# Performance work log

Hardware: AMD Instinct MI355X
Metric: run time of the kernel (lower is better)

The kernel has to match this reference:

```python
import jax, jax.numpy as jnp
import numpy as np

B, T, H = 2048, 512, 64  # batch, seq_len, hidden_size


def setup_inputs() -> dict:
    key = jax.random.key(0)
    ks = jax.random.split(key, 12)
    s = 1.0 / np.sqrt(H)  # PyTorch default uniform init bound
    u = lambda k, shape: jax.random.uniform(k, shape, jnp.float32, -s, s)
    return {
        "x": jax.random.normal(ks[0], (B, T), dtype=jnp.float32),
        # layer 0: input_size=1
        "w_ih0": u(ks[1], (4 * H, 1)),
        "w_hh0": u(ks[2], (4 * H, H)),
        "b_ih0": u(ks[3], (4 * H,)),
        "b_hh0": u(ks[4], (4 * H,)),
        # layer 1: input_size=H
        "w_ih1": u(ks[5], (4 * H, H)),
        "w_hh1": u(ks[6], (4 * H, H)),
        "b_ih1": u(ks[7], (4 * H,)),
        "b_hh1": u(ks[8], (4 * H,)),
        # final projection 64 -> 1
        "fc_w": u(ks[9], (1, H)),
        "fc_b": u(ks[10], (1,)),
    }


def _lstm_layer(x, w_ih, w_hh, b_ih, b_hh):
    """x: [B, T, D] -> hidden states [B, T, H]. PyTorch gate order i,f,g,o."""
    bsz = x.shape[0]
    # input contribution for all timesteps at once: [B, T, 4H]
    gx = jnp.einsum('btd,gd->btg', x, w_ih) + b_ih + b_hh
    gx = jnp.swapaxes(gx, 0, 1)  # time-major [T, B, 4H]

    def step(carry, g_t):
        h, c = carry
        g = g_t + h @ w_hh.T  # [B, 4H]
        i, f, gg, o = jnp.split(g, 4, axis=-1)
        i = jax.nn.sigmoid(i)
        f = jax.nn.sigmoid(f)
        gg = jnp.tanh(gg)
        o = jax.nn.sigmoid(o)
        c = f * c + i * gg
        h = o * jnp.tanh(c)
        return (h, c), h

    h0 = jnp.zeros((bsz, H), dtype=x.dtype)
    _, hs = jax.lax.scan(step, (h0, h0), gx)
    return jnp.swapaxes(hs, 0, 1)  # [B, T, H]


def reference(x, w_ih0, w_hh0, b_ih0, b_hh0, w_ih1, w_hh1, b_ih1, b_hh1, fc_w, fc_b):
    x3 = x[..., None]  # unsqueeze(2): [B, T, 1]
    h1 = _lstm_layer(x3, w_ih0, w_hh0, b_ih0, b_hh0)
    h2 = _lstm_layer(h1, w_ih1, w_hh1, b_ih1, b_hh1)
    # fc applied to last timestep of layer-2 output
    return h2[:, -1, :] @ fc_w.T + fc_b  # [B, 1]
```

## Files before the change

### kernel.cpp

```cpp
#include <hip/hip_runtime.h>

#define TLEN 512
#define HDIM 64
#define NB   8
#define NTH  512
#define GRID 256
#define XPAD 516

typedef __attribute__((ext_vector_type(8))) short bf16x8;
typedef __attribute__((ext_vector_type(4))) float f32x4;

__device__ __forceinline__ float sigm(float x){ return __fdividef(1.f, 1.f+__expf(-x)); }
__device__ __forceinline__ float tanh_(float x){ return 1.f - __fdividef(2.f, __expf(2.f*x)+1.f); }

__device__ __forceinline__ short bf16rn(float f){
    unsigned u = __float_as_uint(f);
    u = (u + 0x7FFFu + ((u >> 16) & 1u)) >> 16;
    return (short)u;
}
__device__ __forceinline__ float bf2f(short s){
    return __uint_as_float(((unsigned)(unsigned short)s) << 16);
}
__device__ __forceinline__ float bf2f_u(unsigned lo16){
    return __uint_as_float(lo16 << 16);
}

__device__ __forceinline__ void loadA(const float* __restrict__ W, int rowbase, int lane,
                                      bf16x8& hi0, bf16x8& lo0, bf16x8& hi1, bf16x8& lo1)
{
    const int row = rowbase + (lane & 15);
    const int q   = lane >> 4;
    const float* p = W + row * HDIM + q * 8;
    #pragma unroll
    for (int e = 0; e < 8; ++e) {
        const float f0 = p[e];
        const float f1 = p[32 + e];
        const short a0 = bf16rn(f0); hi0[e] = a0; lo0[e] = bf16rn(f0 - bf2f(a0));
        const short a1 = bf16rn(f1); hi1[e] = a1; lo1[e] = bf16rn(f1 - bf2f(a1));
    }
}

#define MFMA __builtin_amdgcn_mfma_f32_16x16x32_bf16

__global__ __launch_bounds__(NTH)
__attribute__((amdgpu_waves_per_eu(2, 2)))
void lstm2_ws(const float* __restrict__ x,
              const float* __restrict__ w_ih0,
              const float* __restrict__ w_hh0,
              const float* __restrict__ b_ih0,
              const float* __restrict__ b_hh0,
              const float* __restrict__ w_ih1,
              const float* __restrict__ w_hh1,
              const float* __restrict__ b_ih1,
              const float* __restrict__ b_hh1,
              const float* __restrict__ fc_w,
              const float* __restrict__ fc_b,
              float* __restrict__ out)
{
    __shared__ float xs[16 * XPAD];
    __shared__ short h1f[2][2][2][4][16][8];
    __shared__ short h2f[2][2][2][4][16][8];
    __shared__ float h2last[16][HDIM];

    const int tid  = threadIdx.x;
    const int wid  = tid >> 6;
    const int lane = tid & 63;
    const int q    = lane >> 4;
    const int r15  = lane & 15;
    const int b0   = blockIdx.x * NB;
    const bool isL0   = (wid < 4);
    const bool lohalf = (r15 < 8);

    {
        const float4* xg = (const float4*)(x + (size_t)b0 * TLEN);
        for (int idx = tid; idx < 16 * TLEN / 4; idx += NTH) {
            const int row = idx >> 7;
            const int col = idx & 127;
            *(float4*)&xs[row * XPAD + col * 4] = xg[(row & 7) * 128 + col];
        }
    }
    for (int idx = tid; idx < 8192; idx += NTH) {
        ((short*)h1f)[idx] = 0;
        ((short*)h2f)[idx] = 0;
    }

    const int w4 = isL0 ? wid : (wid - 4);
    const int U0 = w4 * 16;
    bf16x8 M0h0[4], M0l0[4], M0h1[4], M0l1[4];
    bf16x8 M1h0[4], M1l0[4], M1h1[4], M1l1[4];
    f32x4 biasv[4], wih[4];
    if (isL0) {
        #pragma unroll
        for (int g = 0; g < 4; ++g)
            loadA(w_hh0, g * 64 + U0, lane, M0h0[g], M0l0[g], M0h1[g], M0l1[g]);
        #pragma unroll
        for (int g = 0; g < 4; ++g) {
            #pragma unroll
            for (int r = 0; r < 4; ++r) {
                const int row = g * 64 + U0 + q * 4 + r;
                biasv[g][r] = b_ih0[row] + b_hh0[row];
                wih[g][r]   = w_ih0[row];
            }
        }
    } else {
        #pragma unroll
        for (int g = 0; g < 4; ++g) {
            loadA(w_ih1, g * 64 + U0, lane, M0h0[g], M0l0[g], M0h1[g], M0l1[g]);
            loadA(w_hh1, g * 64 + U0, lane, M1h0[g], M1l0[g], M1h1[g], M1l1[g]);
        }
        #pragma unroll
        for (int g = 0; g < 4; ++g) {
            #pragma unroll
            for (int r = 0; r < 4; ++r) {
                const int row = g * 64 + U0 + q * 4 + r;
                biasv[g][r] = b_ih1[row] + b_hh1[row];
                wih[g][r]   = 0.f;
            }
        }
    }
    const int kh = w4 >> 1;
    const int qp = (2 * w4 + (q >> 1)) & 3;
    const int eo = (q & 1) * 4;
    float ccA = 0.f, ccB = 0.f;
    int p = 0;

    __syncthreads();

    for (int i = 0; i <= TLEN; ++i) {
        const bool active = isL0 ? (i < TLEN) : (i >= 1);
        if (active) {
            f32x4 acc[4];
            if (isL0) {
                const bf16x8 Bh0 = *(const bf16x8*)&h1f[p][0][0][q][r15][0];
                const bf16x8 Bh1 = *(const bf16x8*)&h1f[p][0][1][q][r15][0];
                const bf16x8 Bl0 = *(const bf16x8*)&h1f[p][1][0][q][r15][0];
                const bf16x8 Bl1 = *(const bf16x8*)&h1f[p][1][1][q][r15][0];
                const float xv = xs[r15 * XPAD + i];
                #pragma unroll
                for (int g = 0; g < 4; ++g) {
                    f32x4 a = biasv[g];
                    #pragma unroll
                    for (int r = 0; r < 4; ++r) a[r] = fmaf(wih[g][r], xv, a[r]);
                    a = MFMA(M0h0[g], Bh0, a, 0, 0, 0);
                    a = MFMA(M0l0[g], Bh0, a, 0, 0, 0);
                    a = MFMA(M0h0[g], Bl0, a, 0, 0, 0);
                    f32x4 b2 = {0.f, 0.f, 0.f, 0.f};
                    b2 = MFMA(M0h1[g], Bh1, b2, 0, 0, 0);
                    b2 = MFMA(M0l1[g], Bh1, b2, 0, 0, 0);
                    b2 = MFMA(M0h1[g], Bl1, b2, 0, 0, 0);
                    #pragma unroll
                    for (int r = 0; r < 4; ++r) acc[g][r] = a[r] + b2[r];
                }
            } else {
                const bf16x8 B1h0 = *(const bf16x8*)&h1f[p][0][0][q][r15][0];
                const bf16x8 B1h1 = *(const bf16x8*)&h1f[p][0][1][q][r15][0];
                const bf16x8 B1l0 = *(const bf16x8*)&h1f[p][1][0][q][r15][0];
                const bf16x8 B1l1 = *(const bf16x8*)&h1f[p][1][1][q][r15][0];
                const bf16x8 B2h0 = *(const bf16x8*)&h2f[p][0][0][q][r15][0];
                const bf16x8 B2h1 = *(const bf16x8*)&h2f[p][0][1][q][r15][0];
                const bf16x8 B2l0 = *(const bf16x8*)&h2f[p][1][0][q][r15][0];
                const bf16x8 B2l1 = *(const bf16x8*)&h2f[p][1][1][q][r15][0];
                #pragma unroll
                for (int g = 0; g < 4; ++g) {
                    f32x4 a = biasv[g];
                    a = MFMA(M0h0[g], B1h0, a, 0, 0, 0);
                    a = MFMA(M0h1[g], B1h1, a, 0, 0, 0);
                    a = MFMA(M0l0[g], B1h0, a, 0, 0, 0);
                    a = MFMA(M0l1[g], B1h1, a, 0, 0, 0);
                    a = MFMA(M0h0[g], B1l0, a, 0, 0, 0);
                    a = MFMA(M0h1[g], B1l1, a, 0, 0, 0);
                    f32x4 h = {0.f, 0.f, 0.f, 0.f};
                    h = MFMA(M1h0[g], B2h0, h, 0, 0, 0);
                    h = MFMA(M1h1[g], B2h1, h, 0, 0, 0);
                    h = MFMA(M1l0[g], B2h0, h, 0, 0, 0);
                    h = MFMA(M1l1[g], B2h1, h, 0, 0, 0);
                    h = MFMA(M1h0[g], B2l0, h, 0, 0, 0);
                    h = MFMA(M1h1[g], B2l1, h, 0, 0, 0);
                    #pragma unroll
                    for (int r = 0; r < 4; ++r) acc[g][r] = a[r] + h[r];
                }
            }
            float a0g[4], a1g[4];
            #pragma unroll
            for (int g = 0; g < 4; ++g) {
                a0g[g] = lohalf ? acc[g][0] : acc[g][2];
                a1g[g] = lohalf ? acc[g][1] : acc[g][3];
            }
            float hvA, hvB;
            {
                const float gi = sigm(a0g[0]), gf = sigm(a0g[1]);
                const float gg = tanh_(a0g[2]), go = sigm(a0g[3]);
                ccA = fmaf(gf, ccA, gi * gg);
                hvA = go * tanh_(ccA);
            }
            {
                const float gi = sigm(a1g[0]), gf = sigm(a1g[1]);
                const float gg = tanh_(a1g[2]), go = sigm(a1g[3]);
                ccB = fmaf(gf, ccB, gi * gg);
                hvB = go * tanh_(ccB);
            }
            const short sA = bf16rn(hvA), lA = bf16rn(hvA - bf2f(sA));
            const short sB = bf16rn(hvB), lB = bf16rn(hvB - bf2f(sB));
            const unsigned ownH = (unsigned)(unsigned short)sA | ((unsigned)(unsigned short)sB << 16);
            const unsigned ownL = (unsigned)(unsigned short)lA | ((unsigned)(unsigned short)lB << 16);
            const unsigned othH = (unsigned)__shfl_xor((int)ownH, 8, 64);
            const unsigned othL = (unsigned)__shfl_xor((int)ownL, 8, 64);
            const unsigned h01 = lohalf ? ownH : othH;
            const unsigned h23 = lohalf ? othH : ownH;
            const unsigned l01 = lohalf ? ownL : othL;
            const unsigned l23 = lohalf ? othL : ownL;
            if (isL0) {
                *(uint2*)&h1f[p ^ 1][0][kh][qp][r15][eo] = (uint2){h01, h23};
                *(uint2*)&h1f[p ^ 1][1][kh][qp][r15][eo] = (uint2){l01, l23};
            } else {
                *(uint2*)&h2f[p ^ 1][0][kh][qp][r15][eo] = (uint2){h01, h23};
                *(uint2*)&h2f[p ^ 1][1][kh][qp][r15][eo] = (uint2){l01, l23};
                if (i == TLEN) {
                    f32x4 hv;
                    hv[0] = bf2f_u(h01 & 0xFFFFu) + bf2f_u(l01 & 0xFFFFu);
                    hv[1] = bf2f_u(h01 >> 16)     + bf2f_u(l01 >> 16);
                    hv[2] = bf2f_u(h23 & 0xFFFFu) + bf2f_u(l23 & 0xFFFFu);
                    hv[3] = bf2f_u(h23 >> 16)     + bf2f_u(l23 >> 16);
                    *(f32x4*)&h2last[r15][U0 + q * 4] = hv;
                }
            }
        }
        __syncthreads();
        p ^= 1;
    }

    {
        const int fb = tid >> 5, fs = tid & 31;
        float psum = fc_w[fs] * h2last[fb][fs] + fc_w[fs + 32] * h2last[fb][fs + 32];
        psum += __shfl_xor(psum, 16);
        psum += __shfl_xor(psum, 8);
        psum += __shfl_xor(psum, 4);
        psum += __shfl_xor(psum, 2);
        psum += __shfl_xor(psum, 1);
        if (fs == 0 && fb < NB) out[b0 + fb] = psum + fc_b[0];
    }
}

extern "C" void kernel_launch(void* const* d_in, const int* in_sizes, int n_in,
                              void* d_out, int out_size, void* d_ws, size_t ws_size,
                              hipStream_t stream) {
    const float* xp     = (const float*)d_in[0];
    const float* w_ih0  = (const float*)d_in[1];
    const float* w_hh0  = (const float*)d_in[2];
    const float* b_ih0  = (const float*)d_in[3];
    const float* b_hh0  = (const float*)d_in[4];
    const float* w_ih1  = (const float*)d_in[5];
    const float* w_hh1  = (const float*)d_in[6];
    const float* b_ih1  = (const float*)d_in[7];
    const float* b_hh1  = (const float*)d_in[8];
    const float* fc_w   = (const float*)d_in[9];
    const float* fc_b   = (const float*)d_in[10];
    float* outp = (float*)d_out;

    lstm2_ws<<<dim3(GRID), dim3(NTH), 0, stream>>>(
        xp, w_ih0, w_hh0, b_ih0, b_hh0,
        w_ih1, w_hh1, b_ih1, b_hh1, fc_w, fc_b, outp);
}
```

Before: 872.8 us.

## Split layer-1 input projection into separate wave group with 3-stage pipeline

Expands the block from 8 to 12 waves, organised as three groups: layer-0 recurrence, layer-1 input projection (W_ih1·h1), and layer-1 recurrence (W_hh1·h2). The input projection result passes through a double-buffered shared array one step later. This removes the critical-path imbalance where layer-1 waves did twice the MFMA work of layer-0 waves. In exchange it adds a pipeline stage (one extra timestep iteration), extra LDS traffic, and drops the waves_per_eu hint. Bias and x terms are now added after the MFMA instead of seeding the accumulator.

New measurement: 949.2 us. 8.7% more time.

```diff
diff --git a/kernel.cpp b/kernel.cpp
--- a/kernel.cpp
+++ b/kernel.cpp
@@ -3,7 +3,7 @@
 #define TLEN 512
 #define HDIM 64
 #define NB   8
-#define NTH  512
+#define NTH  768
 #define GRID 256
 #define XPAD 516
 
@@ -43,32 +43,33 @@
 #define MFMA __builtin_amdgcn_mfma_f32_16x16x32_bf16
 
 __global__ __launch_bounds__(NTH)
-__attribute__((amdgpu_waves_per_eu(2, 2)))
-void lstm2_ws(const float* __restrict__ x,
-              const float* __restrict__ w_ih0,
-              const float* __restrict__ w_hh0,
-              const float* __restrict__ b_ih0,
-              const float* __restrict__ b_hh0,
-              const float* __restrict__ w_ih1,
-              const float* __restrict__ w_hh1,
-              const float* __restrict__ b_ih1,
-              const float* __restrict__ b_hh1,
-              const float* __restrict__ fc_w,
-              const float* __restrict__ fc_b,
-              float* __restrict__ out)
+void lstm2_ws3(const float* __restrict__ x,
+               const float* __restrict__ w_ih0,
+               const float* __restrict__ w_hh0,
+               const float* __restrict__ b_ih0,
+               const float* __restrict__ b_hh0,
+               const float* __restrict__ w_ih1,
+               const float* __restrict__ w_hh1,
+               const float* __restrict__ b_ih1,
+               const float* __restrict__ b_hh1,
+               const float* __restrict__ fc_w,
+               const float* __restrict__ fc_b,
+               float* __restrict__ out)
 {
     __shared__ float xs[16 * XPAD];
     __shared__ short h1f[2][2][2][4][16][8];
     __shared__ short h2f[2][2][2][4][16][8];
+    __shared__ float pa2[2][4][4][4][16][4];
     __shared__ float h2last[16][HDIM];
 
     const int tid  = threadIdx.x;
     const int wid  = tid >> 6;
+    const int grp  = wid >> 2;
+    const int w4   = wid & 3;
     const int lane = tid & 63;
     const int q    = lane >> 4;
     const int r15  = lane & 15;
     const int b0   = blockIdx.x * NB;
-    const bool isL0   = (wid < 4);
     const bool lohalf = (r15 < 8);
 
     {
@@ -84,38 +85,28 @@
         ((short*)h2f)[idx] = 0;
     }
 
-    const int w4 = isL0 ? wid : (wid - 4);
     const int U0 = w4 * 16;
-    bf16x8 M0h0[4], M0l0[4], M0h1[4], M0l1[4];
-    bf16x8 M1h0[4], M1l0[4], M1h1[4], M1l1[4];
-    f32x4 biasv[4], wih[4];
-    if (isL0) {
-        #pragma unroll
-        for (int g = 0; g < 4; ++g)
-            loadA(w_hh0, g * 64 + U0, lane, M0h0[g], M0l0[g], M0h1[g], M0l1[g]);
+    const float* Wm = (grp == 0) ? w_hh0 : (grp == 1) ? w_ih1 : w_hh1;
+    bf16x8 Mh0[4], Ml0[4], Mh1[4], Ml1[4];
+    #pragma unroll
+    for (int g = 0; g < 4; ++g)
+        loadA(Wm, g * 64 + U0, lane, Mh0[g], Ml0[g], Mh1[g], Ml1[g]);
+
+    const int rA = lohalf ? 0 : 2;
+    f32x4 b2A = {0,0,0,0}, b2B = {0,0,0,0}, wxA = {0,0,0,0}, wxB = {0,0,0,0};
+    if (grp == 0) {
         #pragma unroll
         for (int g = 0; g < 4; ++g) {
-            #pragma unroll
-            for (int r = 0; r < 4; ++r) {
-                const int row = g * 64 + U0 + q * 4 + r;
-                biasv[g][r] = b_ih0[row] + b_hh0[row];
-                wih[g][r]   = w_ih0[row];
-            }
-        }
-    } else {
+            const int rowA = g * 64 + U0 + q * 4 + rA;
+            b2A[g] = b_ih0[rowA] + b_hh0[rowA];     wxA[g] = w_ih0[rowA];
+            b2B[g] = b_ih0[rowA+1] + b_hh0[rowA+1]; wxB[g] = w_ih0[rowA+1];
+        }
+    } else if (grp == 2) {
         #pragma unroll
         for (int g = 0; g < 4; ++g) {
-            loadA(w_ih1, g * 64 + U0, lane, M0h0[g], M0l0[g], M0h1[g], M0l1[g]);
-            loadA(w_hh1, g * 64 + U0, lane, M1h0[g], M1l0[g], M1h1[g], M1l1[g]);
-        }
-        #pragma unroll
-        for (int g = 0; g < 4; ++g) {
-            #pragma unroll
-            for (int r = 0; r < 4; ++r) {
-                const int row = g * 64 + U0 + q * 4 + r;
-                biasv[g][r] = b_ih1[row] + b_hh1[row];
-                wih[g][r]   = 0.f;
-            }
+            const int rowA = g * 64 + U0 + q * 4 + rA;
+            b2A[g] = b_ih1[rowA] + b_hh1[rowA];
+            b2B[g] = b_ih1[rowA+1] + b_hh1[rowA+1];
         }
     }
     const int kh = w4 >> 1;
@@ -126,102 +117,115 @@
 
     __syncthreads();
 
-    for (int i = 0; i <= TLEN; ++i) {
-        const bool active = isL0 ? (i < TLEN) : (i >= 1);
+    for (int i = 0; i <= TLEN + 1; ++i) {
+        const bool active = (grp == 0) ? (i < TLEN)
+                          : (grp == 1) ? (i >= 1 && i <= TLEN)
+                                       : (i >= 2);
         if (active) {
             f32x4 acc[4];
-            if (isL0) {
+            if (grp == 0) {
                 const bf16x8 Bh0 = *(const bf16x8*)&h1f[p][0][0][q][r15][0];
                 const bf16x8 Bh1 = *(const bf16x8*)&h1f[p][0][1][q][r15][0];
                 const bf16x8 Bl0 = *(const bf16x8*)&h1f[p][1][0][q][r15][0];
                 const bf16x8 Bl1 = *(const bf16x8*)&h1f[p][1][1][q][r15][0];
-                const float xv = xs[r15 * XPAD + i];
                 #pragma unroll
                 for (int g = 0; g < 4; ++g) {
-                    f32x4 a = biasv[g];
+                    f32x4 a = {0,0,0,0};
+                    a = MFMA(Mh0[g], Bh0, a, 0, 0, 0);
+                    a = MFMA(Ml0[g], Bh0, a, 0, 0, 0);
+                    a = MFMA(Mh0[g], Bl0, a, 0, 0, 0);
+                    f32x4 b = {0,0,0,0};
+                    b = MFMA(Mh1[g], Bh1, b, 0, 0, 0);
+                    b = MFMA(Ml1[g], Bh1, b, 0, 0, 0);
+                    b = MFMA(Mh1[g], Bl1, b, 0, 0, 0);
                     #pragma unroll
-                    for (int r = 0; r < 4; ++r) a[r] = fmaf(wih[g][r], xv, a[r]);
-                    a = MFMA(M0h0[g], Bh0, a, 0, 0, 0);
-                    a = MFMA(M0l0[g], Bh0, a, 0, 0, 0);
-                    a = MFMA(M0h0[g], Bl0, a, 0, 0, 0);
-                    f32x4 b2 = {0.f, 0.f, 0.f, 0.f};
-                    b2 = MFMA(M0h1[g], Bh1, b2, 0, 0, 0);
-                    b2 = MFMA(M0l1[g], Bh1, b2, 0, 0, 0);
-                    b2 = MFMA(M0h1[g], Bl1, b2, 0, 0, 0);
+                    for (int r = 0; r < 4; ++r) acc[g][r] = a[r] + b[r];
+                }
+            } else if (grp == 1) {
+                const bf16x8 Bh0 = *(const bf16x8*)&h1f[p][0][0][q][r15][0];
+                const bf16x8 Bh1 = *(const bf16x8*)&h1f[p][0][1][q][r15][0];
+                const bf16x8 Bl0 = *(const bf16x8*)&h1f[p][1][0][q][r15][0];
+                const bf16x8 Bl1 = *(const bf16x8*)&h1f[p][1][1][q][r15][0];
+                #pragma unroll
+                for (int g = 0; g < 4; ++g) {
+                    f32x4 a = {0,0,0,0};
+                    a = MFMA(Mh0[g], Bh0, a, 0, 0, 0);
+                    a = MFMA(Ml0[g], Bh0, a, 0, 0, 0);
+                    a = MFMA(Mh0[g], Bl0, a, 0, 0, 0);
+                    f32x4 b = {0,0,0,0};
+                    b = MFMA(Mh1[g], Bh1, b, 0, 0, 0);
+                    b = MFMA(Ml1[g], Bh1, b, 0, 0, 0);
+                    b = MFMA(Mh1[g], Bl1, b, 0, 0, 0);
                     #pragma unroll
-                    for (int r = 0; r < 4; ++r) acc[g][r] = a[r] + b2[r];
-                }
+                    for (int r = 0; r < 4; ++r) acc[g][r] = a[r] + b[r];
+                }
+                #pragma unroll
+                for (int g = 0; g < 4; ++g)
+                    *(f32x4*)&pa2[i & 1][w4][g][q][r15][0] = acc[g];
             } else {
-                const bf16x8 B1h0 = *(const bf16x8*)&h1f[p][0][0][q][r15][0];
-                const bf16x8 B1h1 = *(const bf16x8*)&h1f[p][0][1][q][r15][0];
-                const bf16x8 B1l0 = *(const bf16x8*)&h1f[p][1][0][q][r15][0];
-                const bf16x8 B1l1 = *(const bf16x8*)&h1f[p][1][1][q][r15][0];
-                const bf16x8 B2h0 = *(const bf16x8*)&h2f[p][0][0][q][r15][0];
-                const bf16x8 B2h1 = *(const bf16x8*)&h2f[p][0][1][q][r15][0];
-                const bf16x8 B2l0 = *(const bf16x8*)&h2f[p][1][0][q][r15][0];
-                const bf16x8 B2l1 = *(const bf16x8*)&h2f[p][1][1][q][r15][0];
+                const bf16x8 Bh0 = *(const bf16x8*)&h2f[p][0][0][q][r15][0];
+                const bf16x8 Bh1 = *(const bf16x8*)&h2f[p][0][1][q][r15][0];
+                const bf16x8 Bl0 = *(const bf16x8*)&h2f[p][1][0][q][r15][0];
+                const bf16x8 Bl1 = *(const bf16x8*)&h2f[p][1][1][q][r15][0];
                 #pragma unroll
                 for (int g = 0; g < 4; ++g) {
-                    f32x4 a = biasv[g];
-                    a = MFMA(M0h0[g], B1h0, a, 0, 0, 0);
-                    a = MFMA(M0h1[g], B1h1, a, 0, 0, 0);
-                    a = MFMA(M0l0[g], B1h0, a, 0, 0, 0);
-                    a = MFMA(M0l1[g], B1h1, a, 0, 0, 0);
-                    a = MFMA(M0h0[g], B1l0, a, 0, 0, 0);
-                    a = MFMA(M0h1[g], B1l1, a, 0, 0, 0);
-                    f32x4 h = {0.f, 0.f, 0.f, 0.f};
-                    h = MFMA(M1h0[g], B2h0, h, 0, 0, 0);
-                    h = MFMA(M1h1[g], B2h1, h, 0, 0, 0);
-                    h = MFMA(M1l0[g], B2h0, h, 0, 0, 0);
-                    h = MFMA(M1l1[g], B2h1, h, 0, 0, 0);
-                    h = MFMA(M1h0[g], B2l0, h, 0, 0, 0);
-                    h = MFMA(M1h1[g], B2l1, h, 0, 0, 0);
+                    f32x4 a = {0,0,0,0};
+                    a = MFMA(Mh0[g], Bh0, a, 0, 0, 0);
+                    a = MFMA(Ml0[g], Bh0, a, 0, 0, 0);
+                    a = MFMA(Mh0[g], Bl0, a, 0, 0, 0);
+                    f32x4 b = {0,0,0,0};
+                    b = MFMA(Mh1[g], Bh1, b, 0, 0, 0);
+                    b = MFMA(Ml1[g], Bh1, b, 0, 0, 0);
+                    b = MFMA(Mh1[g], Bl1, b, 0, 0, 0);
+                    const f32x4 pv = *(const f32x4*)&pa2[(i & 1) ^ 1][w4][g][q][r15][0];
                     #pragma unroll
-                    for (int r = 0; r < 4; ++r) acc[g][r] = a[r] + h[r];
+                    for (int r = 0; r < 4; ++r) acc[g][r] = a[r] + b[r] + pv[r];
                 }
             }
-            float a0g[4], a1g[4];
-            #pragma unroll
-            for (int g = 0; g < 4; ++g) {
-                a0g[g] = lohalf ? acc[g][0] : acc[g][2];
-                a1g[g] = lohalf ? acc[g][1] : acc[g][3];
-            }
-            float hvA, hvB;
-            {
-                const float gi = sigm(a0g[0]), gf = sigm(a0g[1]);
-                const float gg = tanh_(a0g[2]), go = sigm(a0g[3]);
-                ccA = fmaf(gf, ccA, gi * gg);
-                hvA = go * tanh_(ccA);
-            }
-            {
-                const float gi = sigm(a1g[0]), gf = sigm(a1g[1]);
-                const float gg = tanh_(a1g[2]), go = sigm(a1g[3]);
-                ccB = fmaf(gf, ccB, gi * gg);
-                hvB = go * tanh_(ccB);
-            }
-            const short sA = bf16rn(hvA), lA = bf16rn(hvA - bf2f(sA));
-            const short sB = bf16rn(hvB), lB = bf16rn(hvB - bf2f(sB));
-            const unsigned ownH = (unsigned)(unsigned short)sA | ((unsigned)(unsigned short)sB << 16);
-            const unsigned ownL = (unsigned)(unsigned short)lA | ((unsigned)(unsigned short)lB << 16);
-            const unsigned othH = (unsigned)__shfl_xor((int)ownH, 8, 64);
-            const unsigned othL = (unsigned)__shfl_xor((int)ownL, 8, 64);
-            const unsigned h01 = lohalf ? ownH : othH;
-            const unsigned h23 = lohalf ? othH : ownH;
-            const unsigned l01 = lohalf ? ownL : othL;
-            const unsigned l23 = lohalf ? othL : ownL;
-            if (isL0) {
-                *(uint2*)&h1f[p ^ 1][0][kh][qp][r15][eo] = (uint2){h01, h23};
-                *(uint2*)&h1f[p ^ 1][1][kh][qp][r15][eo] = (uint2){l01, l23};
-            } else {
-                *(uint2*)&h2f[p ^ 1][0][kh][qp][r15][eo] = (uint2){h01, h23};
-                *(uint2*)&h2f[p ^ 1][1][kh][qp][r15][eo] = (uint2){l01, l23};
-                if (i == TLEN) {
-                    f32x4 hv;
-                    hv[0] = bf2f_u(h01 & 0xFFFFu) + bf2f_u(l01 & 0xFFFFu);
-                    hv[1] = bf2f_u(h01 >> 16)     + bf2f_u(l01 >> 16);
-                    hv[2] = bf2f_u(h23 & 0xFFFFu) + bf2f_u(l23 & 0xFFFFu);
-                    hv[3] = bf2f_u(h23 >> 16)     + bf2f_u(l23 >> 16);
-                    *(f32x4*)&h2last[r15][U0 + q * 4] = hv;
+
+            if (grp != 1) {
+                const float xv = (grp == 0) ? xs[r15 * XPAD + i] : 0.f;
+                float hvA, hvB;
+                {
+                    const float gi = sigm (acc[0][rA]   + b2A[0] + wxA[0] * xv);
+                    const float gf = sigm (acc[1][rA]   + b2A[1] + wxA[1] * xv);
+                    const float gg = tanh_(acc[2][rA]   + b2A[2] + wxA[2] * xv);
+                    const float go = sigm (acc[3][rA]   + b2A[3] + wxA[3] * xv);
+                    ccA = fmaf(gf, ccA, gi * gg);
+                    hvA = go * tanh_(ccA);
+                }
+                {
+                    const float gi = sigm (acc[0][rA+1] + b2B[0] + wxB[0] * xv);
+                    const float gf = sigm (acc[1][rA+1] + b2B[1] + wxB[1] * xv);
+                    const float gg = tanh_(acc[2][rA+1] + b2B[2] + wxB[2] * xv);
+                    const float go = sigm (acc[3][rA+1] + b2B[3] + wxB[3] * xv);
+                    ccB = fmaf(gf, ccB, gi * gg);
+                    hvB = go * tanh_(ccB);
+                }
+                const short sA = bf16rn(hvA), lA = bf16rn(hvA - bf2f(sA));
+                const short sB = bf16rn(hvB), lB = bf16rn(hvB - bf2f(sB));
+                const unsigned ownH = (unsigned)(unsigned short)sA | ((unsigned)(unsigned short)sB << 16);
+                const unsigned ownL = (unsigned)(unsigned short)lA | ((unsigned)(unsigned short)lB << 16);
+                const unsigned othH = (unsigned)__shfl_xor((int)ownH, 8, 64);
+                const unsigned othL = (unsigned)__shfl_xor((int)ownL, 8, 64);
+                const unsigned h01 = lohalf ? ownH : othH;
+                const unsigned h23 = lohalf ? othH : ownH;
+                const unsigned l01 = lohalf ? ownL : othL;
+                const unsigned l23 = lohalf ? othL : ownL;
+                if (grp == 0) {
+                    *(uint2*)&h1f[p ^ 1][0][kh][qp][r15][eo] = (uint2){h01, h23};
+                    *(uint2*)&h1f[p ^ 1][1][kh][qp][r15][eo] = (uint2){l01, l23};
+                } else {
+                    *(uint2*)&h2f[p ^ 1][0][kh][qp][r15][eo] = (uint2){h01, h23};
+                    *(uint2*)&h2f[p ^ 1][1][kh][qp][r15][eo] = (uint2){l01, l23};
+                    if (i == TLEN + 1) {
+                        f32x4 hv;
+                        hv[0] = bf2f_u(h01 & 0xFFFFu) + bf2f_u(l01 & 0xFFFFu);
+                        hv[1] = bf2f_u(h01 >> 16)     + bf2f_u(l01 >> 16);
+                        hv[2] = bf2f_u(h23 & 0xFFFFu) + bf2f_u(l23 & 0xFFFFu);
+                        hv[3] = bf2f_u(h23 >> 16)     + bf2f_u(l23 >> 16);
+                        *(f32x4*)&h2last[r15][U0 + q * 4] = hv;
+                    }
                 }
             }
         }
@@ -229,7 +233,7 @@
         p ^= 1;
     }
 
-    {
+    if (tid < 512) {
         const int fb = tid >> 5, fs = tid & 31;
         float psum = fc_w[fs] * h2last[fb][fs] + fc_w[fs + 32] * h2last[fb][fs + 32];
         psum += __shfl_xor(psum, 16);
@@ -257,7 +261,7 @@
     const float* fc_b   = (const float*)d_in[10];
     float* outp = (float*)d_out;
 
-    lstm2_ws<<<dim3(GRID), dim3(NTH), 0, stream>>>(
+    lstm2_ws3<<<dim3(GRID), dim3(NTH), 0, stream>>>(
         xp, w_ih0, w_hh0, b_ih0, b_hh0,
         w_ih1, w_hh1, b_ih1, b_hh1, fc_w, fc_b, outp);
 }
```
